# Kernel tuning notes

Measured on AMD Instinct MI355X. Metric: run time of the kernel, lower is better.

The kernel has to match this reference:

```python
import jax, jax.numpy as jnp
import numpy as np

B, N, DIM = 4, 2048, 1024
HEAD = 16
INTER = 1024
HD = INTER // HEAD  # 64
SCALE = INTER ** (-0.5)


def setup_inputs() -> dict:
    key = jax.random.key(0)
    k1, k2, k3 = jax.random.split(key, 3)
    features = jax.random.normal(k1, (B, N, DIM), dtype=jnp.float32)
    W_qkv = jax.random.normal(k2, (DIM, 3 * INTER), dtype=jnp.float32) * (DIM ** -0.5)
    W_out = jax.random.normal(k3, (INTER, DIM), dtype=jnp.float32) * (INTER ** -0.5)
    return {"features": features, "W_qkv": W_qkv, "W_out": W_out}


def reference(features, W_qkv, W_out):
    # fc_qkv: [b, n, 3*inter], chunk into q, k, v
    qkv = jnp.einsum('bnd,de->bne', features, W_qkv)
    q, k, v = jnp.split(qkv, 3, axis=-1)
    # b n (h d) -> b n h d
    q = q.reshape(B, N, HEAD, HD)
    k = k.reshape(B, N, HEAD, HD)
    v = v.reshape(B, N, HEAD, HD)
    # scores: b h i j  (scale = inter_dim ** -0.5, as in source)
    alpha = jnp.einsum('bihd,bjhd->bhij', q, k) * SCALE
    att = jax.nn.softmax(alpha, axis=-1)
    out = jnp.einsum('bhij,bjhd->bihd', att, v)
    out = out.reshape(B, N, INTER)
    # fc_out (dropout_ratio=0.0 -> identity)
    return jnp.einsum('bni,id->bnd', out, W_out)
```

## Files before the change

kernel.cpp:

```cpp
#include <hip/hip_runtime.h>
#include <stdint.h>

#define BB 4
#define SEQ 2048
#define DMODEL 1024
#define NHEAD 16
#define HDIM 64
#define INTER 1024
#define QSCALE 0.045084220027780106f

#if __has_builtin(__builtin_amdgcn_exp2f)
#define EXP2F(x) __builtin_amdgcn_exp2f(x)
#else
#define EXP2F(x) exp2f(x)
#endif

typedef unsigned short u16;
typedef __attribute__((ext_vector_type(4))) unsigned short u16x4;
typedef __attribute__((ext_vector_type(4))) short s16x4;
typedef __attribute__((ext_vector_type(8))) short s16x8;
typedef __attribute__((ext_vector_type(4))) float f32x4;
typedef __attribute__((ext_vector_type(16))) float f32x16;

__device__ __forceinline__ u16 f2bf(float f) {
  unsigned int u = __float_as_uint(f);
  u += 0x7FFFu + ((u >> 16) & 1u);
  return (u16)(u >> 16);
}

__device__ __forceinline__ void async16(const u16* g, u16* l) {
  __builtin_amdgcn_global_load_lds((__attribute__((address_space(1))) void*)(void*)(g),
                                   (__attribute__((address_space(3))) void*)(l),
                                   16, 0, 0);
}

__global__ void cast_f32_bf16(const float* __restrict__ src, u16* __restrict__ dst, int n) {
  int i = (blockIdx.x * 256 + threadIdx.x) * 4;
  if (i >= n) return;
  f32x4 v = *reinterpret_cast<const f32x4*>(src + i);
  u16x4 o;
  o[0] = f2bf(v[0]); o[1] = f2bf(v[1]); o[2] = f2bf(v[2]); o[3] = f2bf(v[3]);
  *reinterpret_cast<u16x4*>(dst + i) = o;
}

__global__ void transpose_cast(const float* __restrict__ src, u16* __restrict__ dst,
                               int rows, int cols) {
  __shared__ float tile[32][33];
  int c0 = blockIdx.x * 32, r0 = blockIdx.y * 32;
  int tx = threadIdx.x, ty = threadIdx.y;
  #pragma unroll
  for (int i = ty; i < 32; i += 8) tile[i][tx] = src[(size_t)(r0 + i) * cols + c0 + tx];
  __syncthreads();
  #pragma unroll
  for (int i = ty; i < 32; i += 8)
    dst[(size_t)(c0 + i) * rows + r0 + tx] = f2bf(tile[tx][i]);
}

template <int MODE>
__global__ __launch_bounds__(256, 2) void gemm_bt(
    const u16* __restrict__ A, const u16* __restrict__ BT,
    float* __restrict__ Cf, u16* __restrict__ Qb, u16* __restrict__ Kp,
    u16* __restrict__ Vp, int K, int ldc) {
  __shared__ u16 As[128 * 32];
  __shared__ u16 Bs[128 * 32];
  const int tid = threadIdx.x;
  const int wave = tid >> 6, lane = tid & 63;
  const int row0 = blockIdx.y * 128, col0 = blockIdx.x * 128;
  const int wr = (wave >> 1) * 64, wc = (wave & 1) * 64;
  const int r = lane & 15, q8 = (lane >> 4) * 8;

  f32x4 acc[4][4] = {};

  const int sRow = lane >> 2, sK = (lane & 3) * 8;
  const u16* Ag0 = A + (size_t)(row0 + wave * 32 + sRow) * K + sK;
  const u16* Ag1 = Ag0 + (size_t)16 * K;
  const u16* Bg0 = BT + (size_t)(col0 + wave * 32 + sRow) * K + sK;
  const u16* Bg1 = Bg0 + (size_t)16 * K;
  u16* Al0 = &As[wave * 1024];
  u16* Al1 = Al0 + 512;
  u16* Bl0 = &Bs[wave * 1024];
  u16* Bl1 = Bl0 + 512;

  for (int k0 = 0; k0 < K; k0 += 32) {
    async16(Ag0 + k0, Al0);
    async16(Ag1 + k0, Al1);
    async16(Bg0 + k0, Bl0);
    async16(Bg1 + k0, Bl1);
    __syncthreads();
    s16x8 af[4], bf[4];
    #pragma unroll
    for (int t = 0; t < 4; t++) {
      af[t] = *reinterpret_cast<const s16x8*>(&As[(wr + t * 16 + r) * 32 + q8]);
      bf[t] = *reinterpret_cast<const s16x8*>(&Bs[(wc + t * 16 + r) * 32 + q8]);
    }
    #pragma unroll
    for (int i = 0; i < 4; i++)
      #pragma unroll
      for (int j = 0; j < 4; j++)
        acc[i][j] = __builtin_amdgcn_mfma_f32_16x16x32_bf16(af[i], bf[j], acc[i][j], 0, 0, 0);
    __syncthreads();
  }

  #pragma unroll
  for (int i = 0; i < 4; i++) {
    #pragma unroll
    for (int j = 0; j < 4; j++) {
      #pragma unroll
      for (int reg = 0; reg < 4; reg++) {
        int gr = row0 + wr + i * 16 + (lane >> 4) * 4 + reg;
        int gc = col0 + wc + j * 16 + r;
        float v = acc[i][j][reg];
        if (MODE == 0) {
          int b = gr >> 11, n = gr & (SEQ - 1);
          if (gc < INTER) {
            Qb[(size_t)gr * INTER + gc] = f2bf(v * QSCALE);
          } else if (gc < 2 * INTER) {
            int dim = gc - INTER;
            int h = dim >> 6, d = dim & 63;
            int bh = b * NHEAD + h;
            size_t idx = (((size_t)(bh * 64 + (n >> 5)) * 4 + (d >> 4)) * 64 +
                          ((((d >> 3) & 1) << 5) | (n & 31))) * 8 + (d & 7);
            Kp[idx] = f2bf(v);
          } else {
            int dim = gc - 2 * INTER;
            int h = dim >> 6, d = dim & 63;
            int bh = b * NHEAD + h;
            size_t idx = ((((size_t)(bh * 64 + (n >> 5)) * 2 + ((n >> 4) & 1)) * 2 +
                           (d >> 5)) * 64 +
                          ((((n >> 3) & 1) << 5) | (d & 31))) * 8 + (n & 7);
            Vp[idx] = f2bf(v);
          }
        } else {
          Cf[(size_t)gr * ldc + gc] = v;
        }
      }
    }
  }
}

__global__ __launch_bounds__(256, 4) void attn_kernel(
    const u16* __restrict__ Qb, const u16* __restrict__ Kp,
    const u16* __restrict__ Vp, u16* __restrict__ AO) {
  __shared__ __align__(16) u16 Ps[4][32 * 36];
  const int tid = threadIdx.x;
  const int wave = tid >> 6, lane = tid & 63;
  const int l31 = lane & 31, half = lane >> 5;
  const int bh = blockIdx.x, b = bh >> 4, h = bh & 15;
  const int i0 = blockIdx.y * 128 + wave * 32;

  const u16* qbase = Qb + (size_t)(b * SEQ + i0 + l31) * INTER + h * HDIM + half * 8;
  s16x8 qf[4];
  #pragma unroll
  for (int c = 0; c < 4; c++) qf[c] = *reinterpret_cast<const s16x8*>(qbase + c * 16);

  const u16* kpb = Kp + (size_t)bh * (64 * 4 * 512) + lane * 8;
  const u16* vpb = Vp + (size_t)bh * (64 * 4 * 512) + lane * 8;
  u16* Pw = &Ps[wave][0];

  f32x16 ot0 = {}, ot1 = {};
  float ls = 0.f;

  s16x8 kf[4];
  #pragma unroll
  for (int c = 0; c < 4; c++)
    kf[c] = *reinterpret_cast<const s16x8*>(kpb + c * 512);

  for (int jb = 0; jb < 64; jb++) {
    const int jn = (jb + 1) & 63;
    s16x8 kn[4];
    #pragma unroll
    for (int c = 0; c < 4; c++)
      kn[c] = *reinterpret_cast<const s16x8*>(kpb + jn * 2048 + c * 512);
    s16x8 vf[4];
    #pragma unroll
    for (int c = 0; c < 4; c++)
      vf[c] = *reinterpret_cast<const s16x8*>(vpb + jb * 2048 + c * 512);

    f32x16 st = {};
    #pragma unroll
    for (int c = 0; c < 4; c++)
      st = __builtin_amdgcn_mfma_f32_32x32x16_bf16(kf[c], qf[c], st, 0, 0, 0);

    #pragma unroll
    for (int q = 0; q < 4; q++) {
      u16x4 pk;
      #pragma unroll
      for (int t = 0; t < 4; t++) {
        float p = EXP2F(st[q * 4 + t]);
        ls += p;
        pk[t] = f2bf(p);
      }
      *reinterpret_cast<u16x4*>(&Pw[l31 * 36 + q * 8 + half * 4]) = pk;
    }

    __threadfence_block();

    #pragma unroll
    for (int kc = 0; kc < 2; kc++) {
      const u16* pp = &Pw[l31 * 36 + half * 8 + kc * 16];
      s16x4 plo = *reinterpret_cast<const s16x4*>(pp);
      s16x4 phi = *reinterpret_cast<const s16x4*>(pp + 4);
      s16x8 pb = __builtin_shufflevector(plo, phi, 0, 1, 2, 3, 4, 5, 6, 7);
      ot0 = __builtin_amdgcn_mfma_f32_32x32x16_bf16(vf[kc * 2 + 0], pb, ot0, 0, 0, 0);
      ot1 = __builtin_amdgcn_mfma_f32_32x32x16_bf16(vf[kc * 2 + 1], pb, ot1, 0, 0, 0);
    }

    #pragma unroll
    for (int c = 0; c < 4; c++) kf[c] = kn[c];
  }

  ls += __shfl_xor(ls, 32, 64);
  float rinv = 1.0f / ls;

  u16* orow = AO + (size_t)(b * SEQ + i0 + l31) * INTER + h * HDIM;
  #pragma unroll
  for (int dt = 0; dt < 2; dt++) {
    const f32x16& o = dt ? ot1 : ot0;
    #pragma unroll
    for (int q = 0; q < 4; q++) {
      u16x4 pk;
      #pragma unroll
      for (int t = 0; t < 4; t++) pk[t] = f2bf(o[q * 4 + t] * rinv);
      *reinterpret_cast<u16x4*>(orow + dt * 32 + q * 8 + half * 4) = pk;
    }
  }
}

extern "C" void kernel_launch(void* const* d_in, const int* in_sizes, int n_in,
                              void* d_out, int out_size, void* d_ws, size_t ws_size,
                              hipStream_t stream) {
  const float* features = (const float*)d_in[0];
  const float* W_qkv    = (const float*)d_in[1];
  const float* W_out    = (const float*)d_in[2];
  float* out = (float*)d_out;
  char* w = (char*)d_ws;
  u16* Xb    = (u16*)(w);
  u16* WqkvT = (u16*)(w + 16777216);
  u16* WoutT = (u16*)(w + 23068672);
  u16* Qb    = (u16*)(w + 25165824);
  u16* Kp    = (u16*)(w + 41943040);
  u16* Vp    = (u16*)(w + 58720256);
  u16* AO    = (u16*)(w + 75497472);

  cast_f32_bf16<<<dim3(8192), dim3(256), 0, stream>>>(features, Xb, BB * SEQ * DMODEL);
  transpose_cast<<<dim3(96, 32), dim3(32, 8), 0, stream>>>(W_qkv, WqkvT, DMODEL, 3 * INTER);
  transpose_cast<<<dim3(32, 32), dim3(32, 8), 0, stream>>>(W_out, WoutT, INTER, DMODEL);
  gemm_bt<0><<<dim3(24, 64), dim3(256), 0, stream>>>(Xb, WqkvT, nullptr, Qb, Kp, Vp,
                                                     DMODEL, 0);
  attn_kernel<<<dim3(64, 16), dim3(256), 0, stream>>>(Qb, Kp, Vp, AO);
  gemm_bt<1><<<dim3(8, 64), dim3(256), 0, stream>>>(AO, WoutT, out, nullptr, nullptr,
                                                    nullptr, INTER, DMODEL);
}
```

Measured before the change: 294.8 us.

## Fuse prep kernels, pack bf16 conversions, shrink attention blocks, unroll KV loop

```diff
diff --git a/kernel.cpp b/kernel.cpp
--- a/kernel.cpp
+++ b/kernel.cpp
@@ -28,32 +28,56 @@
   return (u16)(u >> 16);
 }
 
+#if __has_builtin(__builtin_amdgcn_cvt_pk_bf16_f32)
+typedef __attribute__((ext_vector_type(2))) __bf16 bf16x2_t;
+__device__ __forceinline__ unsigned int pk2bf(float a, float b) {
+  bf16x2_t r = __builtin_amdgcn_cvt_pk_bf16_f32(a, b);
+  return *reinterpret_cast<unsigned int*>(&r);
+}
+#else
+__device__ __forceinline__ unsigned int pk2bf(float a, float b) {
+  return (unsigned int)f2bf(a) | ((unsigned int)f2bf(b) << 16);
+}
+#endif
+
 __device__ __forceinline__ void async16(const u16* g, u16* l) {
   __builtin_amdgcn_global_load_lds((__attribute__((address_space(1))) void*)(void*)(g),
                                    (__attribute__((address_space(3))) void*)(l),
                                    16, 0, 0);
 }
 
-__global__ void cast_f32_bf16(const float* __restrict__ src, u16* __restrict__ dst, int n) {
-  int i = (blockIdx.x * 256 + threadIdx.x) * 4;
-  if (i >= n) return;
-  f32x4 v = *reinterpret_cast<const f32x4*>(src + i);
-  u16x4 o;
-  o[0] = f2bf(v[0]); o[1] = f2bf(v[1]); o[2] = f2bf(v[2]); o[3] = f2bf(v[3]);
-  *reinterpret_cast<u16x4*>(dst + i) = o;
-}
-
-__global__ void transpose_cast(const float* __restrict__ src, u16* __restrict__ dst,
-                               int rows, int cols) {
+__global__ __launch_bounds__(256) void prep(
+    const float* __restrict__ f, const float* __restrict__ wqkv,
+    const float* __restrict__ wout, u16* __restrict__ Xb,
+    u16* __restrict__ WqkvT, u16* __restrict__ WoutT) {
   __shared__ float tile[32][33];
-  int c0 = blockIdx.x * 32, r0 = blockIdx.y * 32;
-  int tx = threadIdx.x, ty = threadIdx.y;
-  #pragma unroll
-  for (int i = ty; i < 32; i += 8) tile[i][tx] = src[(size_t)(r0 + i) * cols + c0 + tx];
-  __syncthreads();
-  #pragma unroll
-  for (int i = ty; i < 32; i += 8)
-    dst[(size_t)(c0 + i) * rows + r0 + tx] = f2bf(tile[tx][i]);
+  const int bid = blockIdx.x, tid = threadIdx.x;
+  if (bid < 8192) {
+    int i = (bid * 256 + tid) * 4;
+    f32x4 v = *reinterpret_cast<const f32x4*>(f + i);
+    uint2 o;
+    o.x = pk2bf(v[0], v[1]);
+    o.y = pk2bf(v[2], v[3]);
+    *reinterpret_cast<uint2*>(Xb + i) = o;
+  } else {
+    const float* src; u16* dst; int rows, cols, bx, by;
+    if (bid < 8192 + 3072) {
+      int t = bid - 8192;
+      src = wqkv; dst = WqkvT; rows = DMODEL; cols = 3 * INTER;
+      bx = t % 96; by = t / 96;
+    } else {
+      int t = bid - 11264;
+      src = wout; dst = WoutT; rows = INTER; cols = DMODEL;
+      bx = t & 31; by = t >> 5;
+    }
+    int c0 = bx * 32, r0 = by * 32, tx = tid & 31, ty = tid >> 5;
+    #pragma unroll
+    for (int i = ty; i < 32; i += 8) tile[i][tx] = src[(size_t)(r0 + i) * cols + c0 + tx];
+    __syncthreads();
+    #pragma unroll
+    for (int i = ty; i < 32; i += 8)
+      dst[(size_t)(c0 + i) * rows + r0 + tx] = f2bf(tile[tx][i]);
+  }
 }
 
 template <int MODE>
@@ -101,52 +125,90 @@
     __syncthreads();
   }
 
+  const int quad = lane >> 4;
   #pragma unroll
   for (int i = 0; i < 4; i++) {
+    const int n = row0 + wr + i * 16 + quad * 4;
+    const int b = n >> 11, nn = n & (SEQ - 1);
     #pragma unroll
     for (int j = 0; j < 4; j++) {
-      #pragma unroll
-      for (int reg = 0; reg < 4; reg++) {
-        int gr = row0 + wr + i * 16 + (lane >> 4) * 4 + reg;
-        int gc = col0 + wc + j * 16 + r;
-        float v = acc[i][j][reg];
-        if (MODE == 0) {
-          int b = gr >> 11, n = gr & (SEQ - 1);
-          if (gc < INTER) {
-            Qb[(size_t)gr * INTER + gc] = f2bf(v * QSCALE);
-          } else if (gc < 2 * INTER) {
-            int dim = gc - INTER;
-            int h = dim >> 6, d = dim & 63;
-            int bh = b * NHEAD + h;
-            size_t idx = (((size_t)(bh * 64 + (n >> 5)) * 4 + (d >> 4)) * 64 +
-                          ((((d >> 3) & 1) << 5) | (n & 31))) * 8 + (d & 7);
-            Kp[idx] = f2bf(v);
-          } else {
-            int dim = gc - 2 * INTER;
-            int h = dim >> 6, d = dim & 63;
-            int bh = b * NHEAD + h;
-            size_t idx = ((((size_t)(bh * 64 + (n >> 5)) * 2 + ((n >> 4) & 1)) * 2 +
-                           (d >> 5)) * 64 +
-                          ((((n >> 3) & 1) << 5) | (d & 31))) * 8 + (n & 7);
-            Vp[idx] = f2bf(v);
-          }
-        } else {
-          Cf[(size_t)gr * ldc + gc] = v;
-        }
+      const int gc = col0 + wc + j * 16 + r;
+      if (MODE == 1) {
+        #pragma unroll
+        for (int reg = 0; reg < 4; reg++)
+          Cf[(size_t)(n + reg) * ldc + gc] = acc[i][j][reg];
+      } else if (gc < INTER) {
+        size_t base = (size_t)n * INTER + gc;
+        #pragma unroll
+        for (int reg = 0; reg < 4; reg++)
+          Qb[base + (size_t)reg * INTER] = f2bf(acc[i][j][reg] * QSCALE);
+      } else if (gc < 2 * INTER) {
+        int dim = gc - INTER, h = dim >> 6, d = dim & 63;
+        int bh = b * NHEAD + h;
+        size_t base = (((size_t)(bh * 64 + (nn >> 5)) * 4 + (d >> 4)) * 64 +
+                       ((((d >> 3) & 1) << 5) | (nn & 31))) * 8 + (d & 7);
+        #pragma unroll
+        for (int reg = 0; reg < 4; reg++)
+          Kp[base + reg * 8] = f2bf(acc[i][j][reg]);
+      } else {
+        int dim = gc - 2 * INTER, h = dim >> 6, d = dim & 63;
+        int bh = b * NHEAD + h;
+        size_t base = ((((size_t)(bh * 64 + (nn >> 5)) * 2 + ((nn >> 4) & 1)) * 2 +
+                        (d >> 5)) * 64 +
+                       ((((nn >> 3) & 1) << 5) | (d & 31))) * 8 + (nn & 7);
+        uint2 pk;
+        pk.x = pk2bf(acc[i][j][0], acc[i][j][1]);
+        pk.y = pk2bf(acc[i][j][2], acc[i][j][3]);
+        *reinterpret_cast<uint2*>(Vp + base) = pk;
       }
     }
   }
 }
 
-__global__ __launch_bounds__(256, 4) void attn_kernel(
+#define ATTN_STEP(JCUR, KC, KN)                                                   \
+  {                                                                               \
+    const int jnext = ((JCUR) + 1) & 63;                                          \
+    _Pragma("unroll")                                                             \
+    for (int c = 0; c < 4; c++)                                                   \
+      KN[c] = *reinterpret_cast<const s16x8*>(kpb + jnext * 2048 + c * 512);      \
+    s16x8 vf[4];                                                                  \
+    _Pragma("unroll")                                                             \
+    for (int c = 0; c < 4; c++)                                                   \
+      vf[c] = *reinterpret_cast<const s16x8*>(vpb + (JCUR) * 2048 + c * 512);     \
+    f32x16 st = {};                                                               \
+    _Pragma("unroll")                                                             \
+    for (int c = 0; c < 4; c++)                                                   \
+      st = __builtin_amdgcn_mfma_f32_32x32x16_bf16(KC[c], qf[c], st, 0, 0, 0);    \
+    _Pragma("unroll")                                                             \
+    for (int q = 0; q < 4; q++) {                                                 \
+      float p0 = EXP2F(st[q * 4 + 0]), p1 = EXP2F(st[q * 4 + 1]);                 \
+      float p2 = EXP2F(st[q * 4 + 2]), p3 = EXP2F(st[q * 4 + 3]);                 \
+      ls += (p0 + p1) + (p2 + p3);                                                \
+      uint2 pk;                                                                   \
+      pk.x = pk2bf(p0, p1);                                                       \
+      pk.y = pk2bf(p2, p3);                                                       \
+      *reinterpret_cast<uint2*>(&Pw[l31 * 36 + q * 8 + half * 4]) = pk;           \
+    }                                                                             \
+    _Pragma("unroll")                                                             \
+    for (int kc = 0; kc < 2; kc++) {                                              \
+      const u16* pp = &Pw[l31 * 36 + half * 8 + kc * 16];                         \
+      s16x4 plo = *reinterpret_cast<const s16x4*>(pp);                            \
+      s16x4 phi = *reinterpret_cast<const s16x4*>(pp + 4);                        \
+      s16x8 pb = __builtin_shufflevector(plo, phi, 0, 1, 2, 3, 4, 5, 6, 7);       \
+      ot0 = __builtin_amdgcn_mfma_f32_32x32x16_bf16(vf[kc * 2 + 0], pb, ot0, 0, 0, 0); \
+      ot1 = __builtin_amdgcn_mfma_f32_32x32x16_bf16(vf[kc * 2 + 1], pb, ot1, 0, 0, 0); \
+    }                                                                             \
+  }
+
+__global__ __launch_bounds__(128, 4) void attn_kernel(
     const u16* __restrict__ Qb, const u16* __restrict__ Kp,
     const u16* __restrict__ Vp, u16* __restrict__ AO) {
-  __shared__ __align__(16) u16 Ps[4][32 * 36];
+  __shared__ __align__(16) u16 Ps[2][32 * 36];
   const int tid = threadIdx.x;
   const int wave = tid >> 6, lane = tid & 63;
   const int l31 = lane & 31, half = lane >> 5;
   const int bh = blockIdx.x, b = bh >> 4, h = bh & 15;
-  const int i0 = blockIdx.y * 128 + wave * 32;
+  const int i0 = blockIdx.y * 64 + wave * 32;
 
   const u16* qbase = Qb + (size_t)(b * SEQ + i0 + l31) * INTER + h * HDIM + half * 8;
   s16x8 qf[4];
@@ -160,53 +222,14 @@
   f32x16 ot0 = {}, ot1 = {};
   float ls = 0.f;
 
-  s16x8 kf[4];
+  s16x8 kf0[4], kf1[4];
   #pragma unroll
   for (int c = 0; c < 4; c++)
-    kf[c] = *reinterpret_cast<const s16x8*>(kpb + c * 512);
-
-  for (int jb = 0; jb < 64; jb++) {
-    const int jn = (jb + 1) & 63;
-    s16x8 kn[4];
-    #pragma unroll
-    for (int c = 0; c < 4; c++)
-      kn[c] = *reinterpret_cast<const s16x8*>(kpb + jn * 2048 + c * 512);
-    s16x8 vf[4];
-    #pragma unroll
-    for (int c = 0; c < 4; c++)
-      vf[c] = *reinterpret_cast<const s16x8*>(vpb + jb * 2048 + c * 512);
-
-    f32x16 st = {};
-    #pragma unroll
-    for (int c = 0; c < 4; c++)
-      st = __builtin_amdgcn_mfma_f32_32x32x16_bf16(kf[c], qf[c], st, 0, 0, 0);
-
-    #pragma unroll
-    for (int q = 0; q < 4; q++) {
-      u16x4 pk;
-      #pragma unroll
-      for (int t = 0; t < 4; t++) {
-        float p = EXP2F(st[q * 4 + t]);
-        ls += p;
-        pk[t] = f2bf(p);
-      }
-      *reinterpret_cast<u16x4*>(&Pw[l31 * 36 + q * 8 + half * 4]) = pk;
-    }
-
-    __threadfence_block();
-
-    #pragma unroll
-    for (int kc = 0; kc < 2; kc++) {
-      const u16* pp = &Pw[l31 * 36 + half * 8 + kc * 16];
-      s16x4 plo = *reinterpret_cast<const s16x4*>(pp);
-      s16x4 phi = *reinterpret_cast<const s16x4*>(pp + 4);
-      s16x8 pb = __builtin_shufflevector(plo, phi, 0, 1, 2, 3, 4, 5, 6, 7);
-      ot0 = __builtin_amdgcn_mfma_f32_32x32x16_bf16(vf[kc * 2 + 0], pb, ot0, 0, 0, 0);
-      ot1 = __builtin_amdgcn_mfma_f32_32x32x16_bf16(vf[kc * 2 + 1], pb, ot1, 0, 0, 0);
-    }
-
-    #pragma unroll
-    for (int c = 0; c < 4; c++) kf[c] = kn[c];
+    kf0[c] = *reinterpret_cast<const s16x8*>(kpb + c * 512);
+
+  for (int jb = 0; jb < 64; jb += 2) {
+    ATTN_STEP(jb, kf0, kf1)
+    ATTN_STEP(jb + 1, kf1, kf0)
   }
 
   ls += __shfl_xor(ls, 32, 64);
@@ -218,10 +241,10 @@
     const f32x16& o = dt ? ot1 : ot0;
     #pragma unroll
     for (int q = 0; q < 4; q++) {
-      u16x4 pk;
-      #pragma unroll
-      for (int t = 0; t < 4; t++) pk[t] = f2bf(o[q * 4 + t] * rinv);
-      *reinterpret_cast<u16x4*>(orow + dt * 32 + q * 8 + half * 4) = pk;
+      uint2 pk;
+      pk.x = pk2bf(o[q * 4 + 0] * rinv, o[q * 4 + 1] * rinv);
+      pk.y = pk2bf(o[q * 4 + 2] * rinv, o[q * 4 + 3] * rinv);
+      *reinterpret_cast<uint2*>(orow + dt * 32 + q * 8 + half * 4) = pk;
     }
   }
 }
@@ -242,12 +265,10 @@
   u16* Vp    = (u16*)(w + 58720256);
   u16* AO    = (u16*)(w + 75497472);
 
-  cast_f32_bf16<<<dim3(8192), dim3(256), 0, stream>>>(features, Xb, BB * SEQ * DMODEL);
-  transpose_cast<<<dim3(96, 32), dim3(32, 8), 0, stream>>>(W_qkv, WqkvT, DMODEL, 3 * INTER);
-  transpose_cast<<<dim3(32, 32), dim3(32, 8), 0, stream>>>(W_out, WoutT, INTER, DMODEL);
+  prep<<<dim3(12288), dim3(256), 0, stream>>>(features, W_qkv, W_out, Xb, WqkvT, WoutT);
   gemm_bt<0><<<dim3(24, 64), dim3(256), 0, stream>>>(Xb, WqkvT, nullptr, Qb, Kp, Vp,
                                                      DMODEL, 0);
-  attn_kernel<<<dim3(64, 16), dim3(256), 0, stream>>>(Qb, Kp, Vp, AO);
+  attn_kernel<<<dim3(64, 32), dim3(128), 0, stream>>>(Qb, Kp, Vp, AO);
   gemm_bt<1><<<dim3(8, 64), dim3(256), 0, stream>>>(AO, WoutT, out, nullptr, nullptr,
                                                     nullptr, INTER, DMODEL);
 }
```

After: 278.2 us. -5.6%, faster.
